# Kernel optimization log

Measured on AMD Instinct MI355X. Metric: run time of the kernel, lower is better.

## Reference

```python
import jax, jax.numpy as jnp
import numpy as np

N_NODES = 50000
N_EDGES = 800000
D_IN = 512
D_OUT = 512


def setup_inputs() -> dict:
    key = jax.random.key(0)
    k1, k2, k3, k4, k5 = jax.random.split(key, 5)
    x = jax.random.normal(k1, (N_NODES, D_IN), dtype=jnp.float32)
    weight = jax.random.normal(k2, (D_IN, D_OUT), dtype=jnp.float32) * (1.0 / np.sqrt(D_IN))
    edge_weight = jax.random.uniform(k3, (N_EDGES,), dtype=jnp.float32)
    edge_src = jax.random.randint(k4, (N_EDGES,), 0, N_NODES, dtype=jnp.int32)
    edge_dst = jax.random.randint(k5, (N_EDGES,), 0, N_NODES, dtype=jnp.int32)
    return {"x": x, "weight": weight, "edge_weight": edge_weight,
            "edge_src": edge_src, "edge_dst": edge_dst}


def reference(x, weight, edge_weight, edge_src, edge_dst):
    # support = x @ W  (dense GEMM, [N, D_out])
    support = jnp.matmul(x, weight)
    # output = adj @ support  (SpMM in COO form):
    # gather source rows, scale by edge weight, scatter-add into destinations
    msgs = support[edge_src] * edge_weight[:, None]          # [E, D_out]
    output = jax.ops.segment_sum(msgs, edge_dst, num_segments=N_NODES)
    return output
```

## Files before the change

kernel.cpp:

```cpp
#include <hip/hip_runtime.h>
#include <stdint.h>

#define N_NODES 50000
#define N_EDGES 800000
#define D 512
#define M_PAD 50048
#define CAP 64
#define CAPSH 6

#define FILL_NB 3125
#define WT_NB   1024
#define GEMM_NB 1564

typedef __attribute__((ext_vector_type(8))) __bf16 bf16x8;
typedef __attribute__((ext_vector_type(8))) unsigned short u16x8;
typedef __attribute__((ext_vector_type(4))) float f32x4;

static __device__ __forceinline__ unsigned short f2bf(float f) {
  unsigned u = __float_as_uint(f);
  u += 0x7fff + ((u >> 16) & 1);
  return (unsigned short)(u >> 16);
}
static __device__ __forceinline__ float bf2f(unsigned short h) {
  return __uint_as_float(((unsigned)h) << 16);
}

static __device__ __forceinline__ void gload_lds16(const void* g, void* l) {
  __builtin_amdgcn_global_load_lds((const __attribute__((address_space(1))) unsigned*)g,
                                   (__attribute__((address_space(3))) unsigned*)l, 16, 0, 0);
}

__global__ __launch_bounds__(256) void k_mega(const float* __restrict__ w,
                                              const float* __restrict__ ew,
                                              const int* __restrict__ esrc,
                                              const int* __restrict__ edst,
                                              unsigned short* __restrict__ wt,
                                              int* __restrict__ cur,
                                              int2* __restrict__ cew) {
  int bid = blockIdx.x;
  if (bid < FILL_NB) {
    int e = bid * 256 + threadIdx.x;
    int d = edst[e];
    int r = atomicAdd(&cur[d], 1);
    if (r < CAP) cew[(d << CAPSH) + r] = make_int2(esrc[e], __float_as_int(ew[e]));
    return;
  }
  bid -= FILL_NB;
  int n = bid >> 1;
  int k = ((bid & 1) << 8) + threadIdx.x;
  wt[n * D + k] = f2bf(w[k * D + n]);
}

__global__ __launch_bounds__(256) void k_gemm(const float* __restrict__ X,
                                              const unsigned short* __restrict__ Bt,
                                              unsigned short* __restrict__ C) {
  __shared__ unsigned short lds_a[128 * 64];
  __shared__ unsigned short lds_b[128 * 64];

  const int orig = blockIdx.x;
  const int q = GEMM_NB / 8, rq = GEMM_NB % 8;
  const int xcd = orig & 7, jj0 = orig >> 3;
  const int wgid = (xcd < rq ? xcd * (q + 1) : rq * (q + 1) + (xcd - rq) * q) + jj0;
  const int bm = wgid >> 2, bn = wgid & 3;

  const int tid  = threadIdx.x;
  const int m0   = bm * 128, n0 = bn * 128;
  const int wave = tid >> 6, lane = tid & 63;
  const int wm   = wave & 1, wn = wave >> 1;
  const int l15  = lane & 15, quad = lane >> 4;

  f32x4 acc[4][4];
#pragma unroll
  for (int i = 0; i < 4; i++)
#pragma unroll
    for (int j = 0; j < 4; j++) acc[i][j] = f32x4{0.f, 0.f, 0.f, 0.f};

  for (int kt = 0; kt < D / 64; ++kt) {
    const int k0 = kt * 64;
    __syncthreads();
#pragma unroll
    for (int c = 0; c < 4; c++) {
      int i = c * 256 + wave * 64 + lane;
      int r = i >> 3, s = i & 7;
      int g = s ^ (r & 7);
      gload_lds16(&Bt[(long long)(n0 + r) * D + k0 + (g << 3)], &lds_b[(c * 256 + wave * 64) * 8]);
      int arow = m0 + r;
      u16x8 val = {0, 0, 0, 0, 0, 0, 0, 0};
      if (arow < N_NODES) {
        const float* src = X + (long long)arow * D + k0 + (g << 3);
        float4 lo = *(const float4*)src;
        float4 hi = *(const float4*)(src + 4);
        val[0] = f2bf(lo.x); val[1] = f2bf(lo.y); val[2] = f2bf(lo.z); val[3] = f2bf(lo.w);
        val[4] = f2bf(hi.x); val[5] = f2bf(hi.y); val[6] = f2bf(hi.z); val[7] = f2bf(hi.w);
      }
      *(u16x8*)&lds_a[(c * 256 + wave * 64 + lane) * 8] = val;
    }
    __syncthreads();
#pragma unroll
    for (int kk = 0; kk < 2; kk++) {
      bf16x8 af[4], bfr[4];
#pragma unroll
      for (int t = 0; t < 4; t++) {
        int ra = wm * 64 + t * 16 + l15;
        int rb = wn * 64 + t * 16 + l15;
        af[t]  = *(const bf16x8*)&lds_a[ra * 64 + ((((kk << 2) + quad) ^ (ra & 7)) << 3)];
        bfr[t] = *(const bf16x8*)&lds_b[rb * 64 + ((((kk << 2) + quad) ^ (rb & 7)) << 3)];
      }
#pragma unroll
      for (int i = 0; i < 4; i++)
#pragma unroll
        for (int j = 0; j < 4; j++)
          acc[i][j] = __builtin_amdgcn_mfma_f32_16x16x32_bf16(af[i], bfr[j], acc[i][j], 0, 0, 0);
    }
  }

#pragma unroll
  for (int i = 0; i < 4; i++)
#pragma unroll
    for (int j = 0; j < 4; j++)
#pragma unroll
      for (int r = 0; r < 4; r++) {
        int row = m0 + wm * 64 + i * 16 + quad * 4 + r;
        int col = n0 + wn * 64 + j * 16 + l15;
        C[(long long)row * D + col] = f2bf(acc[i][j][r]);
      }
}

__global__ __launch_bounds__(256) void k_agg(const int* __restrict__ cur,
                                             const int2* __restrict__ cew,
                                             const unsigned short* __restrict__ S,
                                             float* __restrict__ out) {
  __shared__ float s_part[4 * 512];
  const int node  = blockIdx.x;
  int cnt = cur[node];
  cnt = (cnt > CAP) ? CAP : cnt;
  const int start = node << CAPSH, end = start + cnt;
  const int wave  = threadIdx.x >> 6, lane = threadIdx.x & 63;
  float a[8];
#pragma unroll
  for (int k = 0; k < 8; k++) a[k] = 0.f;

#define EDGE_FMA(V, W)                                             \
  do {                                                             \
    a[0] = fmaf(W, bf2f((unsigned short)(V.x & 0xffffu)), a[0]);   \
    a[1] = fmaf(W, bf2f((unsigned short)(V.x >> 16)),     a[1]);   \
    a[2] = fmaf(W, bf2f((unsigned short)(V.y & 0xffffu)), a[2]);   \
    a[3] = fmaf(W, bf2f((unsigned short)(V.y >> 16)),     a[3]);   \
    a[4] = fmaf(W, bf2f((unsigned short)(V.z & 0xffffu)), a[4]);   \
    a[5] = fmaf(W, bf2f((unsigned short)(V.z >> 16)),     a[5]);   \
    a[6] = fmaf(W, bf2f((unsigned short)(V.w & 0xffffu)), a[6]);   \
    a[7] = fmaf(W, bf2f((unsigned short)(V.w >> 16)),     a[7]);   \
  } while (0)

#define GATHER(P) (*(const uint4*)(S + (size_t)(P).x * D + lane * 8))

  int e = start + wave;
  for (; e + 4 < end; e += 8) {
    int2 p0 = cew[e], p1 = cew[e + 4];
    uint4 v0 = GATHER(p0);
    uint4 v1 = GATHER(p1);
    EDGE_FMA(v0, __int_as_float(p0.y));
    EDGE_FMA(v1, __int_as_float(p1.y));
  }
  if (e < end) {
    int2 p0 = cew[e];
    uint4 v0 = GATHER(p0);
    EDGE_FMA(v0, __int_as_float(p0.y));
  }
#undef GATHER
#undef EDGE_FMA

  float4* sp = (float4*)&s_part[wave * 512 + lane * 8];
  sp[0] = make_float4(a[0], a[1], a[2], a[3]);
  sp[1] = make_float4(a[4], a[5], a[6], a[7]);
  __syncthreads();
  int col = threadIdx.x * 2;
  float2 r0 = *(const float2*)&s_part[0 * 512 + col];
  float2 r1 = *(const float2*)&s_part[1 * 512 + col];
  float2 r2 = *(const float2*)&s_part[2 * 512 + col];
  float2 r3 = *(const float2*)&s_part[3 * 512 + col];
  float2 res = make_float2(r0.x + r1.x + r2.x + r3.x, r0.y + r1.y + r2.y + r3.y);
  typedef __attribute__((ext_vector_type(2))) float f32x2;
  f32x2 rv = {res.x, res.y};
  __builtin_nontemporal_store(rv, (f32x2*)(out + (size_t)node * D + col));
}

extern "C" void kernel_launch(void* const* d_in, const int* in_sizes, int n_in,
                              void* d_out, int out_size, void* d_ws, size_t ws_size,
                              hipStream_t stream) {
  const float* x    = (const float*)d_in[0];
  const float* w    = (const float*)d_in[1];
  const float* ew   = (const float*)d_in[2];
  const int*   esrc = (const int*)d_in[3];
  const int*   edst = (const int*)d_in[4];
  float* out = (float*)d_out;

  char* p = (char*)d_ws;
  auto align256 = [](size_t v) { return (v + 255) & ~(size_t)255; };
  unsigned short* sb = (unsigned short*)p;  p += align256((size_t)M_PAD * D * 2);
  unsigned short* wt = (unsigned short*)p;  p += align256((size_t)D * D * 2);
  int*   cur  = (int*)p;   p += align256((size_t)N_NODES * 4);
  int2*  cew  = (int2*)p;  p += align256((size_t)N_NODES * CAP * 8);

  hipMemsetAsync(cur, 0, (size_t)N_NODES * 4, stream);
  k_mega<<<FILL_NB + WT_NB, 256, 0, stream>>>(w, ew, esrc, edst, wt, cur, cew);
  k_gemm<<<GEMM_NB, 256, 0, stream>>>(x, wt, sb);
  k_agg<<<N_NODES, 256, 0, stream>>>(cur, cew, sb, out);
}
```

Baseline: 397.6 us.

## Fuse edge-bucketing into GEMM launch and load fp32 A tiles directly to LDS

Replaces the memset with zeroing inside a new pre-kernel that also transposes W, and moves the COO bucket fill into the GEMM launch as extra blocks so it overlaps with the matrix multiply. The GEMM now streams fp32 X tiles straight into LDS with global_load_lds and converts to bf16 when reading fragments, instead of converting in registers before the LDS store. This removes one launch and one memset and lets the bucketing hide behind GEMM work. The cost is double the LDS footprint for A (which may lower occupancy), conversion work repeated on every fragment read, and fill blocks that now hold the GEMM's large shared allocation.

```diff
diff --git a/kernel.cpp b/kernel.cpp
--- a/kernel.cpp
+++ b/kernel.cpp
@@ -8,12 +8,11 @@
 #define CAP 64
 #define CAPSH 6
 
-#define FILL_NB 3125
 #define WT_NB   1024
 #define GEMM_NB 1564
+#define FILL_NB 3125
 
 typedef __attribute__((ext_vector_type(8))) __bf16 bf16x8;
-typedef __attribute__((ext_vector_type(8))) unsigned short u16x8;
 typedef __attribute__((ext_vector_type(4))) float f32x4;
 
 static __device__ __forceinline__ unsigned short f2bf(float f) {
@@ -30,32 +29,34 @@
                                    (__attribute__((address_space(3))) unsigned*)l, 16, 0, 0);
 }
 
-__global__ __launch_bounds__(256) void k_mega(const float* __restrict__ w,
-                                              const float* __restrict__ ew,
-                                              const int* __restrict__ esrc,
-                                              const int* __restrict__ edst,
-                                              unsigned short* __restrict__ wt,
-                                              int* __restrict__ cur,
-                                              int2* __restrict__ cew) {
-  int bid = blockIdx.x;
-  if (bid < FILL_NB) {
-    int e = bid * 256 + threadIdx.x;
+__global__ __launch_bounds__(256) void k_pre(const float* __restrict__ w,
+                                             unsigned short* __restrict__ wt,
+                                             int* __restrict__ cur) {
+  int t = blockIdx.x * 256 + threadIdx.x;
+  if (t < N_NODES) cur[t] = 0;
+  int n = blockIdx.x >> 1;
+  int k = ((blockIdx.x & 1) << 8) + threadIdx.x;
+  wt[n * D + k] = f2bf(w[k * D + n]);
+}
+
+__global__ __launch_bounds__(256) void k_gf(const float* __restrict__ X,
+                                            const unsigned short* __restrict__ Bt,
+                                            unsigned short* __restrict__ C,
+                                            const float* __restrict__ ew,
+                                            const int* __restrict__ esrc,
+                                            const int* __restrict__ edst,
+                                            int* __restrict__ cur,
+                                            int2* __restrict__ cew) {
+  __shared__ float          lds_af[128 * 64];
+  __shared__ unsigned short lds_b [128 * 64];
+
+  if (blockIdx.x >= GEMM_NB) {
+    int e = (blockIdx.x - GEMM_NB) * 256 + threadIdx.x;
     int d = edst[e];
     int r = atomicAdd(&cur[d], 1);
     if (r < CAP) cew[(d << CAPSH) + r] = make_int2(esrc[e], __float_as_int(ew[e]));
     return;
   }
-  bid -= FILL_NB;
-  int n = bid >> 1;
-  int k = ((bid & 1) << 8) + threadIdx.x;
-  wt[n * D + k] = f2bf(w[k * D + n]);
-}
-
-__global__ __launch_bounds__(256) void k_gemm(const float* __restrict__ X,
-                                              const unsigned short* __restrict__ Bt,
-                                              unsigned short* __restrict__ C) {
-  __shared__ unsigned short lds_a[128 * 64];
-  __shared__ unsigned short lds_b[128 * 64];
 
   const int orig = blockIdx.x;
   const int q = GEMM_NB / 8, rq = GEMM_NB % 8;
@@ -84,16 +85,15 @@
       int r = i >> 3, s = i & 7;
       int g = s ^ (r & 7);
       gload_lds16(&Bt[(long long)(n0 + r) * D + k0 + (g << 3)], &lds_b[(c * 256 + wave * 64) * 8]);
+    }
+#pragma unroll
+    for (int c = 0; c < 8; c++) {
+      int i = c * 256 + wave * 64 + lane;
+      int r = i >> 4, s = i & 15;
+      int g = s ^ (r & 15);
       int arow = m0 + r;
-      u16x8 val = {0, 0, 0, 0, 0, 0, 0, 0};
-      if (arow < N_NODES) {
-        const float* src = X + (long long)arow * D + k0 + (g << 3);
-        float4 lo = *(const float4*)src;
-        float4 hi = *(const float4*)(src + 4);
-        val[0] = f2bf(lo.x); val[1] = f2bf(lo.y); val[2] = f2bf(lo.z); val[3] = f2bf(lo.w);
-        val[4] = f2bf(hi.x); val[5] = f2bf(hi.y); val[6] = f2bf(hi.z); val[7] = f2bf(hi.w);
-      }
-      *(u16x8*)&lds_a[(c * 256 + wave * 64 + lane) * 8] = val;
+      arow = (arow < N_NODES) ? arow : (N_NODES - 1);
+      gload_lds16(&X[(long long)arow * D + k0 + (g << 2)], &lds_af[(c * 256 + wave * 64) * 4]);
     }
     __syncthreads();
 #pragma unroll
@@ -102,8 +102,15 @@
 #pragma unroll
       for (int t = 0; t < 4; t++) {
         int ra = wm * 64 + t * 16 + l15;
+        int ma = ra & 15;
+        int c0 = kk * 8 + quad * 2;
+        f32x4 lo = *(const f32x4*)&lds_af[ra * 64 + ((c0 ^ ma) << 2)];
+        f32x4 hi = *(const f32x4*)&lds_af[ra * 64 + (((c0 + 1) ^ ma) << 2)];
+        bf16x8 a;
+        a[0] = (__bf16)lo[0]; a[1] = (__bf16)lo[1]; a[2] = (__bf16)lo[2]; a[3] = (__bf16)lo[3];
+        a[4] = (__bf16)hi[0]; a[5] = (__bf16)hi[1]; a[6] = (__bf16)hi[2]; a[7] = (__bf16)hi[3];
+        af[t] = a;
         int rb = wn * 64 + t * 16 + l15;
-        af[t]  = *(const bf16x8*)&lds_a[ra * 64 + ((((kk << 2) + quad) ^ (ra & 7)) << 3)];
         bfr[t] = *(const bf16x8*)&lds_b[rb * 64 + ((((kk << 2) + quad) ^ (rb & 7)) << 3)];
       }
 #pragma unroll
@@ -202,8 +209,7 @@
   int*   cur  = (int*)p;   p += align256((size_t)N_NODES * 4);
   int2*  cew  = (int2*)p;  p += align256((size_t)N_NODES * CAP * 8);
 
-  hipMemsetAsync(cur, 0, (size_t)N_NODES * 4, stream);
-  k_mega<<<FILL_NB + WT_NB, 256, 0, stream>>>(w, ew, esrc, edst, wt, cur, cew);
-  k_gemm<<<GEMM_NB, 256, 0, stream>>>(x, wt, sb);
+  k_pre<<<WT_NB, 256, 0, stream>>>(w, wt, cur);
+  k_gf<<<GEMM_NB + FILL_NB, 256, 0, stream>>>(x, wt, sb, ew, esrc, edst, cur, cew);
   k_agg<<<N_NODES, 256, 0, stream>>>(cur, cew, sb, out);
 }
```

Measured after the change: 353.2 us (median of 2 runs). -11.2%, faster.
